# Performance work log

Measured on AMD Instinct MI355X. Metric: run time of the kernel, lower is better.

The kernel has to match this reference:

```python
import jax, jax.numpy as jnp
import numpy as np

HEAD_SIZE = 16
HIDDEN = 1024
NEG_INF = -1e9


def setup_inputs() -> dict:
    key = jax.random.key(0)
    ks = jax.random.split(key, 9)
    B, S, H = 2, 2048, HIDDEN
    q = jax.random.normal(ks[0], (B, S, H), dtype=jnp.float32)
    k = jax.random.normal(ks[1], (B, S, H), dtype=jnp.float32)
    v = jax.random.normal(ks[2], (B, S, H), dtype=jnp.float32)
    mask = jnp.ones((B, S), dtype=jnp.int32)
    scale = 1.0 / np.sqrt(H)
    wq = jax.random.normal(ks[3], (H, H), dtype=jnp.float32) * scale
    bq = jnp.zeros((H,), dtype=jnp.float32)
    wk = jax.random.normal(ks[4], (H, H), dtype=jnp.float32) * scale
    bk = jnp.zeros((H,), dtype=jnp.float32)
    wv = jax.random.normal(ks[5], (H, H), dtype=jnp.float32) * scale
    bv = jnp.zeros((H,), dtype=jnp.float32)
    return {"q": q, "k": k, "v": v, "mask": mask,
            "wq": wq, "bq": bq, "wk": wk, "bk": bk, "wv": wv, "bv": bv}


def _split_heads(x):
    # [B, S, H] -> [B, n_heads, S, head_dim]
    B, S, H = x.shape
    return x.reshape(B, S, HEAD_SIZE, H // HEAD_SIZE).transpose(0, 2, 1, 3)


def reference(q, k, v, mask, wq, bq, wk, bk, wv, bv):
    B, S, H = q.shape
    qh = _split_heads(q @ wq + bq)  # [B, nH, S, d]
    kh = _split_heads(k @ wk + bk)
    vh = _split_heads(v @ wv + bv)
    # scores scaled by sqrt(hidden_size) -- faithful to original (not head_dim)
    scores = jnp.einsum('bhqd,bhkd->bhqk', qh, kh) / jnp.sqrt(jnp.float32(H))
    # original: mask[0] of shape [B,S] -> [B,1,S,1], masks query rows
    m = mask.astype(jnp.float32)[:, None, :, None]  # [B,1,S,1]
    scores = scores + NEG_INF * (1.0 - m)
    weights = jax.nn.softmax(scores, axis=-1)
    out = jnp.einsum('bhqk,bhkd->bhqd', weights, vh)  # [B, nH, S, d]
    return out.transpose(0, 2, 1, 3).reshape(B, S, H)
```

## Files before the change

### kernel.cpp

```cpp
#include <hip/hip_runtime.h>
#include <hip/hip_bf16.h>
#include <math.h>

typedef __bf16 bf16_t;
typedef __bf16 bf16x8 __attribute__((ext_vector_type(8)));
typedef __bf16 bf16x4 __attribute__((ext_vector_type(4)));
typedef float floatx4 __attribute__((ext_vector_type(4)));

#define QSCALE 0.045084222f

__device__ __forceinline__ void gload_lds16(const bf16_t* g, bf16_t* l) {
  __builtin_amdgcn_global_load_lds(
      (const __attribute__((address_space(1))) void*)(g),
      (__attribute__((address_space(3))) void*)(l), 16, 0, 0);
}

__device__ __forceinline__ float fast_exp2(float x) {
  float r;
  asm("v_exp_f32 %0, %1" : "=v"(r) : "v"(x));
  return r;
}

__global__ __launch_bounds__(256) void transpose3_k(
    const float* __restrict__ wq, const float* __restrict__ wk,
    const float* __restrict__ wv, bf16_t* __restrict__ wt) {
  __shared__ float tile[32][33];
  const float* src = (blockIdx.z == 0) ? wq : (blockIdx.z == 1) ? wk : wv;
  bf16_t* dst = wt + (size_t)blockIdx.z * (1024u * 1024u);
  const int tx = threadIdx.x, ty = threadIdx.y;
  const int x = blockIdx.x * 32 + tx;
  const int y = blockIdx.y * 32 + ty;
#pragma unroll
  for (int i = 0; i < 32; i += 8)
    tile[ty + i][tx] = src[(size_t)(y + i) * 1024 + x];
  __syncthreads();
  const int x2 = blockIdx.y * 32 + tx;
  const int y2 = blockIdx.x * 32 + ty;
#pragma unroll
  for (int i = 0; i < 32; i += 8)
    dst[(size_t)(y2 + i) * 1024 + x2] = (bf16_t)tile[tx][ty + i];
}

__global__ __launch_bounds__(256) void qkv_gemm_k(
    const float* __restrict__ qx, const float* __restrict__ kx,
    const float* __restrict__ vx, const bf16_t* __restrict__ wt3,
    const float* __restrict__ bq, const float* __restrict__ bk,
    const float* __restrict__ bv, bf16_t* __restrict__ Qh,
    bf16_t* __restrict__ Kh, bf16_t* __restrict__ Vt) {
  const int proj = blockIdx.z;
  const float* X = (proj == 0) ? qx : (proj == 1) ? kx : vx;
  const bf16_t* Wt = wt3 + (size_t)proj * (1024u * 1024u);
  const float* bias = (proj == 0) ? bq : (proj == 1) ? bk : bv;

  __shared__ __align__(16) bf16_t As[128 * 64];
  __shared__ __align__(16) bf16_t Bs[128 * 64];

  const int t = threadIdx.x;
  const int lane = t & 63;
  const int w = t >> 6;
  const int wm = (w >> 1) * 64;
  const int wn = (w & 1) * 64;
  const int m0 = blockIdx.x * 128;
  const int n0 = blockIdx.y * 128;
  const int lm = lane & 15;
  const int lq = lane >> 4;

  floatx4 acc[4][4];
#pragma unroll
  for (int i = 0; i < 4; ++i)
#pragma unroll
    for (int j = 0; j < 4; ++j) acc[i][j] = (floatx4){0.f, 0.f, 0.f, 0.f};

  for (int k0 = 0; k0 < 1024; k0 += 64) {
    float4 fa[4][2];
#pragma unroll
    for (int c = 0; c < 4; ++c) {
      const int E = c * 2048 + t * 8;
      const int row = E >> 6;
      const int g = ((E >> 3) & 7) ^ (row & 7);
      const float* src = X + (size_t)(m0 + row) * 1024 + k0 + g * 8;
      fa[c][0] = *(const float4*)(src);
      fa[c][1] = *(const float4*)(src + 4);
    }
    __syncthreads();
#pragma unroll
    for (int c = 0; c < 4; ++c) {
      const int E = c * 2048 + t * 8;
      const int row = E >> 6;
      const int g = ((E >> 3) & 7) ^ (row & 7);
      gload_lds16(Wt + (size_t)(n0 + row) * 1024 + k0 + g * 8, Bs + E);
      bf16x8 hv;
      hv[0] = (bf16_t)fa[c][0].x; hv[1] = (bf16_t)fa[c][0].y;
      hv[2] = (bf16_t)fa[c][0].z; hv[3] = (bf16_t)fa[c][0].w;
      hv[4] = (bf16_t)fa[c][1].x; hv[5] = (bf16_t)fa[c][1].y;
      hv[6] = (bf16_t)fa[c][1].z; hv[7] = (bf16_t)fa[c][1].w;
      *(bf16x8*)(As + E) = hv;
    }
    __syncthreads();

#pragma unroll
    for (int kc = 0; kc < 2; ++kc) {
      bf16x8 a[4], b[4];
#pragma unroll
      for (int i = 0; i < 4; ++i) {
        const int ch = ((kc * 4 + lq) ^ (lm & 7)) * 8;
        a[i] = *(const bf16x8*)(As + (wm + i * 16 + lm) * 64 + ch);
        b[i] = *(const bf16x8*)(Bs + (wn + i * 16 + lm) * 64 + ch);
      }
      if (proj < 2) {
#pragma unroll
        for (int i = 0; i < 4; ++i)
#pragma unroll
          for (int j = 0; j < 4; ++j)
            acc[i][j] = __builtin_amdgcn_mfma_f32_16x16x32_bf16(b[j], a[i],
                                                               acc[i][j], 0, 0, 0);
      } else {
#pragma unroll
        for (int i = 0; i < 4; ++i)
#pragma unroll
          for (int j = 0; j < 4; ++j)
            acc[i][j] = __builtin_amdgcn_mfma_f32_16x16x32_bf16(a[i], b[j],
                                                               acc[i][j], 0, 0, 0);
      }
    }
  }

  if (proj == 2) {
#pragma unroll
    for (int j = 0; j < 4; ++j) {
      const int gn = n0 + wn + j * 16 + lm;
      const float bval = bias[gn];
      const int h = gn >> 6, d = gn & 63;
#pragma unroll
      for (int i = 0; i < 4; ++i) {
        const int gm = m0 + wm + i * 16 + lq * 4;
        const int bb = gm >> 11, s0 = gm & 2047;
        bf16x4 pk;
#pragma unroll
        for (int ii = 0; ii < 4; ++ii) pk[ii] = (bf16_t)(acc[i][j][ii] + bval);
        *(bf16x4*)(Vt + (((size_t)bb * 16 + h) * 64 + d) * 2048 + s0) = pk;
      }
    }
  } else {
    bf16_t* outp = (proj == 0) ? Qh : Kh;
    const float scale = (proj == 0) ? QSCALE : 1.0f;
#pragma unroll
    for (int j = 0; j < 4; ++j) {
      const int nb = n0 + wn + j * 16 + lq * 4;
      float bs4[4];
#pragma unroll
      for (int ii = 0; ii < 4; ++ii) bs4[ii] = bias[nb + ii];
      const int h = nb >> 6, d0 = nb & 63;
#pragma unroll
      for (int i = 0; i < 4; ++i) {
        const int gm = m0 + wm + i * 16 + lm;
        const int bb = gm >> 11, s = gm & 2047;
        bf16x4 pk;
#pragma unroll
        for (int ii = 0; ii < 4; ++ii)
          pk[ii] = (bf16_t)((acc[i][j][ii] + bs4[ii]) * scale);
        *(bf16x4*)(outp + (((size_t)bb * 16 + h) * 2048 + s) * 64 + d0) = pk;
      }
    }
  }
}

__global__ __launch_bounds__(256) void attn_k(
    const bf16_t* __restrict__ Qh, const bf16_t* __restrict__ Kh,
    const bf16_t* __restrict__ Vt, float* __restrict__ out) {
  __shared__ __align__(16) bf16_t Ks[128 * 64];
  __shared__ __align__(16) bf16_t Vs[64 * 128];
  __shared__ __align__(16) bf16_t Ps[4][32 * 128];

  const int t = threadIdx.x;
  const int lane = t & 63;
  const int w = t >> 6;
  const int lm = lane & 15;
  const int lq = lane >> 4;
  const int b = blockIdx.x >> 4, h = blockIdx.x & 15;
  const int q0 = blockIdx.y * 128;
  const size_t bh = (size_t)b * 16 + h;
  const bf16_t* Qb = Qh + bh * (2048 * 64);
  const bf16_t* Kb = Kh + bh * (2048 * 64);
  const bf16_t* Vb = Vt + bh * (64 * 2048);

  bf16x8 qf[2][2];
#pragma unroll
  for (int im = 0; im < 2; ++im)
#pragma unroll
    for (int kc = 0; kc < 2; ++kc)
      qf[im][kc] = *(const bf16x8*)(Qb +
          (size_t)(q0 + w * 32 + im * 16 + lm) * 64 + kc * 32 + lq * 8);

  float lsum[2] = {0.f, 0.f};
  floatx4 accO[2][4];
#pragma unroll
  for (int im = 0; im < 2; ++im)
#pragma unroll
    for (int jd = 0; jd < 4; ++jd) accO[im][jd] = (floatx4){0.f, 0.f, 0.f, 0.f};

  for (int kt = 0; kt < 2048; kt += 128) {
    __syncthreads();
#pragma unroll
    for (int c = 0; c < 4; ++c) {
      const int e = c * 2048 + t * 8;
      const int key = e >> 6, gk = ((e >> 3) & 7) ^ (key & 7);
      gload_lds16(Kb + (size_t)(kt + key) * 64 + gk * 8, Ks + e);
      const int vr = e >> 7, gv = ((e >> 3) & 15) ^ (vr & 15);
      gload_lds16(Vb + (size_t)vr * 2048 + kt + gv * 8, Vs + e);
    }
    __syncthreads();

    floatx4 accS[2][8];
#pragma unroll
    for (int jn = 0; jn < 8; ++jn) {
      const int krow = jn * 16 + lm;
      const bf16x8 k0 = *(const bf16x8*)(Ks + krow * 64 + ((lq) ^ (lm & 7)) * 8);
      const bf16x8 k1 = *(const bf16x8*)(Ks + krow * 64 + ((4 + lq) ^ (lm & 7)) * 8);
#pragma unroll
      for (int im = 0; im < 2; ++im) {
        floatx4 z = {0.f, 0.f, 0.f, 0.f};
        z = __builtin_amdgcn_mfma_f32_16x16x32_bf16(k0, qf[im][0], z, 0, 0, 0);
        z = __builtin_amdgcn_mfma_f32_16x16x32_bf16(k1, qf[im][1], z, 0, 0, 0);
        accS[im][jn] = z;
      }
    }

#pragma unroll
    for (int im = 0; im < 2; ++im) {
      const int pr = im * 16 + lm;
#pragma unroll
      for (int jn = 0; jn < 8; ++jn) {
        bf16x4 pk;
#pragma unroll
        for (int ii = 0; ii < 4; ++ii) {
          const float p = fast_exp2(accS[im][jn][ii]);
          lsum[im] += p;
          pk[ii] = (bf16_t)p;
        }
        const int c2 = ((jn * 2) + (lq >> 1)) ^ lm;
        *(bf16x4*)(Ps[w] + pr * 128 + c2 * 8 + (lq & 1) * 4) = pk;
      }
    }
    asm volatile("s_waitcnt lgkmcnt(0)" ::: "memory");

#pragma unroll
    for (int kc = 0; kc < 4; ++kc) {
      bf16x8 ap[2];
#pragma unroll
      for (int im = 0; im < 2; ++im)
        ap[im] = *(const bf16x8*)(Ps[w] + (im * 16 + lm) * 128 +
                                  ((kc * 4 + lq) ^ lm) * 8);
#pragma unroll
      for (int jd = 0; jd < 4; ++jd) {
        const bf16x8 vf = *(const bf16x8*)(Vs + (jd * 16 + lm) * 128 +
                                           ((kc * 4 + lq) ^ lm) * 8);
#pragma unroll
        for (int im = 0; im < 2; ++im)
          accO[im][jd] =
              __builtin_amdgcn_mfma_f32_16x16x32_bf16(vf, ap[im], accO[im][jd], 0, 0, 0);
      }
    }
  }

  float inv[2];
#pragma unroll
  for (int im = 0; im < 2; ++im) {
    float l = lsum[im];
    l += __shfl_xor(l, 16, 64);
    l += __shfl_xor(l, 32, 64);
    inv[im] = 1.0f / l;
  }

#pragma unroll
  for (int im = 0; im < 2; ++im) {
    const int s = q0 + w * 32 + im * 16 + lm;
    float* op = out + ((size_t)b * 2048 + s) * 1024 + h * 64 + lq * 4;
#pragma unroll
    for (int jd = 0; jd < 4; ++jd) {
      float4 o;
      o.x = accO[im][jd][0] * inv[im];
      o.y = accO[im][jd][1] * inv[im];
      o.z = accO[im][jd][2] * inv[im];
      o.w = accO[im][jd][3] * inv[im];
      *(float4*)(op + jd * 16) = o;
    }
  }
}

extern "C" void kernel_launch(void* const* d_in, const int* in_sizes, int n_in,
                              void* d_out, int out_size, void* d_ws, size_t ws_size,
                              hipStream_t stream) {
  (void)in_sizes; (void)n_in; (void)out_size; (void)ws_size;
  const float* q = (const float*)d_in[0];
  const float* k = (const float*)d_in[1];
  const float* v = (const float*)d_in[2];
  const float* wq = (const float*)d_in[4];
  const float* bq = (const float*)d_in[5];
  const float* wk = (const float*)d_in[6];
  const float* bk = (const float*)d_in[7];
  const float* wv = (const float*)d_in[8];
  const float* bv = (const float*)d_in[9];
  float* out = (float*)d_out;

  bf16_t* ws = (bf16_t*)d_ws;
  bf16_t* Wt = ws;
  bf16_t* Qh = ws + 3u * 1048576u;
  bf16_t* Kh = Qh + 4194304u;
  bf16_t* Vt = Kh + 4194304u;

  transpose3_k<<<dim3(32, 32, 3), dim3(32, 8, 1), 0, stream>>>(wq, wk, wv, Wt);
  qkv_gemm_k<<<dim3(32, 8, 3), dim3(256, 1, 1), 0, stream>>>(
      q, k, v, Wt, bq, bk, bv, Qh, Kh, Vt);
  attn_k<<<dim3(32, 16, 1), dim3(256, 1, 1), 0, stream>>>(Qh, Kh, Vt, out);
}
```

Baseline: 214.6 us.

## Double-buffer QKV GEMM tiles and register-prefetch K/V in attention loop

The projection GEMM now keeps two LDS buffers for A and B. It prefetches the next B tile by async global-to-LDS and the A tile two steps ahead into registers, so only one barrier is needed per iteration and loads overlap the MFMA work. The attention kernel replaces the direct global-to-LDS K/V loads with a register prefetch of the next tile, which is issued after the LDS store and runs during compute. The cost is twice the LDS in the GEMM and more registers in both kernels, which could lower occupancy.

```diff
diff --git a/kernel.cpp b/kernel.cpp
--- a/kernel.cpp
+++ b/kernel.cpp
@@ -52,8 +52,8 @@
   const bf16_t* Wt = wt3 + (size_t)proj * (1024u * 1024u);
   const float* bias = (proj == 0) ? bq : (proj == 1) ? bk : bv;
 
-  __shared__ __align__(16) bf16_t As[128 * 64];
-  __shared__ __align__(16) bf16_t Bs[128 * 64];
+  __shared__ __align__(16) bf16_t As[2][128 * 64];
+  __shared__ __align__(16) bf16_t Bs[2][128 * 64];
 
   const int t = threadIdx.x;
   const int lane = t & 63;
@@ -65,38 +65,63 @@
   const int lm = lane & 15;
   const int lq = lane >> 4;
 
+  int srow[4], sg[4];
+#pragma unroll
+  for (int c = 0; c < 4; ++c) {
+    const int E = c * 2048 + t * 8;
+    srow[c] = E >> 6;
+    sg[c] = (((E >> 3) & 7) ^ (srow[c] & 7)) * 8;
+  }
+
   floatx4 acc[4][4];
 #pragma unroll
   for (int i = 0; i < 4; ++i)
 #pragma unroll
     for (int j = 0; j < 4; ++j) acc[i][j] = (floatx4){0.f, 0.f, 0.f, 0.f};
 
-  for (int k0 = 0; k0 < 1024; k0 += 64) {
-    float4 fa[4][2];
-#pragma unroll
-    for (int c = 0; c < 4; ++c) {
-      const int E = c * 2048 + t * 8;
-      const int row = E >> 6;
-      const int g = ((E >> 3) & 7) ^ (row & 7);
-      const float* src = X + (size_t)(m0 + row) * 1024 + k0 + g * 8;
-      fa[c][0] = *(const float4*)(src);
-      fa[c][1] = *(const float4*)(src + 4);
-    }
+  float4 fa[2][4][2];
+
+#define LOAD_A(bank, k0)                                                     \
+  {                                                                          \
+    _Pragma("unroll") for (int c = 0; c < 4; ++c) {                          \
+      const float* src = X + (size_t)(m0 + srow[c]) * 1024 + (k0) + sg[c];   \
+      fa[bank][c][0] = *(const float4*)(src);                                \
+      fa[bank][c][1] = *(const float4*)(src + 4);                            \
+    }                                                                        \
+  }
+
+#define GLDS_B(buf, k0)                                                      \
+  {                                                                          \
+    _Pragma("unroll") for (int c = 0; c < 4; ++c) {                          \
+      const int E = c * 2048 + t * 8;                                        \
+      gload_lds16(Wt + (size_t)(n0 + srow[c]) * 1024 + (k0) + sg[c],         \
+                  Bs[buf] + E);                                              \
+    }                                                                        \
+  }
+
+#define CVT_WRITE_A(bank, buf)                                               \
+  {                                                                          \
+    _Pragma("unroll") for (int c = 0; c < 4; ++c) {                          \
+      const int E = c * 2048 + t * 8;                                        \
+      bf16x8 hv;                                                             \
+      hv[0] = (bf16_t)fa[bank][c][0].x; hv[1] = (bf16_t)fa[bank][c][0].y;    \
+      hv[2] = (bf16_t)fa[bank][c][0].z; hv[3] = (bf16_t)fa[bank][c][0].w;    \
+      hv[4] = (bf16_t)fa[bank][c][1].x; hv[5] = (bf16_t)fa[bank][c][1].y;    \
+      hv[6] = (bf16_t)fa[bank][c][1].z; hv[7] = (bf16_t)fa[bank][c][1].w;    \
+      *(bf16x8*)(As[buf] + E) = hv;                                          \
+    }                                                                        \
+  }
+
+  LOAD_A(0, 0);
+  GLDS_B(0, 0);
+  CVT_WRITE_A(0, 0);
+  LOAD_A(1, 64);
+
+  int p = 0;
+  for (int it = 0; it < 16; ++it, p ^= 1) {
     __syncthreads();
-#pragma unroll
-    for (int c = 0; c < 4; ++c) {
-      const int E = c * 2048 + t * 8;
-      const int row = E >> 6;
-      const int g = ((E >> 3) & 7) ^ (row & 7);
-      gload_lds16(Wt + (size_t)(n0 + row) * 1024 + k0 + g * 8, Bs + E);
-      bf16x8 hv;
-      hv[0] = (bf16_t)fa[c][0].x; hv[1] = (bf16_t)fa[c][0].y;
-      hv[2] = (bf16_t)fa[c][0].z; hv[3] = (bf16_t)fa[c][0].w;
-      hv[4] = (bf16_t)fa[c][1].x; hv[5] = (bf16_t)fa[c][1].y;
-      hv[6] = (bf16_t)fa[c][1].z; hv[7] = (bf16_t)fa[c][1].w;
-      *(bf16x8*)(As + E) = hv;
-    }
-    __syncthreads();
+    if (it + 1 < 16) GLDS_B(p ^ 1, (it + 1) * 64);
+    if (it + 2 < 16) LOAD_A(p, (it + 2) * 64);
 
 #pragma unroll
     for (int kc = 0; kc < 2; ++kc) {
@@ -104,8 +129,8 @@
 #pragma unroll
       for (int i = 0; i < 4; ++i) {
         const int ch = ((kc * 4 + lq) ^ (lm & 7)) * 8;
-        a[i] = *(const bf16x8*)(As + (wm + i * 16 + lm) * 64 + ch);
-        b[i] = *(const bf16x8*)(Bs + (wn + i * 16 + lm) * 64 + ch);
+        a[i] = *(const bf16x8*)(As[p] + (wm + i * 16 + lm) * 64 + ch);
+        b[i] = *(const bf16x8*)(Bs[p] + (wn + i * 16 + lm) * 64 + ch);
       }
       if (proj < 2) {
 #pragma unroll
@@ -123,7 +148,11 @@
                                                                acc[i][j], 0, 0, 0);
       }
     }
-  }
+    if (it + 1 < 16) CVT_WRITE_A(p ^ 1, p ^ 1);
+  }
+#undef LOAD_A
+#undef GLDS_B
+#undef CVT_WRITE_A
 
   if (proj == 2) {
 #pragma unroll
@@ -199,17 +228,32 @@
 #pragma unroll
     for (int jd = 0; jd < 4; ++jd) accO[im][jd] = (floatx4){0.f, 0.f, 0.f, 0.f};
 
+  bf16x8 kv[8];
+
+#define LOAD_KV(kt)                                                          \
+  {                                                                          \
+    _Pragma("unroll") for (int c = 0; c < 4; ++c) {                          \
+      const int e = c * 2048 + t * 8;                                        \
+      const int key = e >> 6, gk = ((e >> 3) & 7) ^ (key & 7);               \
+      kv[c] = *(const bf16x8*)(Kb + (size_t)((kt) + key) * 64 + gk * 8);     \
+      const int vr = e >> 7, gv = ((e >> 3) & 15) ^ (vr & 15);               \
+      kv[4 + c] = *(const bf16x8*)(Vb + (size_t)vr * 2048 + (kt) + gv * 8);  \
+    }                                                                        \
+  }
+
+  LOAD_KV(0);
+
   for (int kt = 0; kt < 2048; kt += 128) {
     __syncthreads();
 #pragma unroll
     for (int c = 0; c < 4; ++c) {
       const int e = c * 2048 + t * 8;
-      const int key = e >> 6, gk = ((e >> 3) & 7) ^ (key & 7);
-      gload_lds16(Kb + (size_t)(kt + key) * 64 + gk * 8, Ks + e);
-      const int vr = e >> 7, gv = ((e >> 3) & 15) ^ (vr & 15);
-      gload_lds16(Vb + (size_t)vr * 2048 + kt + gv * 8, Vs + e);
+      *(bf16x8*)(Ks + e) = kv[c];
+      *(bf16x8*)(Vs + e) = kv[4 + c];
     }
     __syncthreads();
+
+    if (kt + 128 < 2048) LOAD_KV(kt + 128);
 
     floatx4 accS[2][8];
 #pragma unroll
@@ -262,6 +306,7 @@
       }
     }
   }
+#undef LOAD_KV
 
   float inv[2];
 #pragma unroll
```

Result: slower. 327.4 us (+52.5%).

## Pre-convert activations to bf16 and register-prefetch K/V tiles in attention

Applied to the files above, without the earlier changes.

Adds a separate kernel that converts the q/k/v activations to bf16 once, so the QKV GEMM can load both operands straight into LDS with direct global-to-LDS loads instead of fp32 loads and per-tile conversion. The attention kernel now prefetches the next K/V tile into registers while computing the current one, then stores it to LDS, replacing the synchronous direct-to-LDS loads. The costs are an extra kernel launch with a full read and write of the activations, plus higher register pressure in the attention kernel.

```diff
diff --git a/kernel.cpp b/kernel.cpp
--- a/kernel.cpp
+++ b/kernel.cpp
@@ -19,6 +19,22 @@
   float r;
   asm("v_exp_f32 %0, %1" : "=v"(r) : "v"(x));
   return r;
+}
+
+__global__ __launch_bounds__(256) void cvt3_k(
+    const float* __restrict__ q, const float* __restrict__ k,
+    const float* __restrict__ v, bf16_t* __restrict__ xb) {
+  const float* src = (blockIdx.y == 0) ? q : (blockIdx.y == 1) ? k : v;
+  bf16_t* dst = xb + (size_t)blockIdx.y * 4194304u;
+  const int i = (blockIdx.x * 256 + threadIdx.x) * 8;
+  float4 f0 = *(const float4*)(src + i);
+  float4 f1 = *(const float4*)(src + i + 4);
+  bf16x8 hv;
+  hv[0] = (bf16_t)f0.x; hv[1] = (bf16_t)f0.y;
+  hv[2] = (bf16_t)f0.z; hv[3] = (bf16_t)f0.w;
+  hv[4] = (bf16_t)f1.x; hv[5] = (bf16_t)f1.y;
+  hv[6] = (bf16_t)f1.z; hv[7] = (bf16_t)f1.w;
+  *(bf16x8*)(dst + i) = hv;
 }
 
 __global__ __launch_bounds__(256) void transpose3_k(
@@ -42,14 +58,13 @@
 }
 
 __global__ __launch_bounds__(256) void qkv_gemm_k(
-    const float* __restrict__ qx, const float* __restrict__ kx,
-    const float* __restrict__ vx, const bf16_t* __restrict__ wt3,
+    const bf16_t* __restrict__ xb3, const bf16_t* __restrict__ wt3,
     const float* __restrict__ bq, const float* __restrict__ bk,
     const float* __restrict__ bv, bf16_t* __restrict__ Qh,
     bf16_t* __restrict__ Kh, bf16_t* __restrict__ Vt) {
   const int proj = blockIdx.z;
-  const float* X = (proj == 0) ? qx : (proj == 1) ? kx : vx;
-  const bf16_t* Wt = wt3 + (size_t)proj * (1024u * 1024u);
+  const bf16_t* X = xb3 + (size_t)proj * 4194304u;
+  const bf16_t* Wt = wt3 + (size_t)proj * 1048576u;
   const float* bias = (proj == 0) ? bq : (proj == 1) ? bk : bv;
 
   __shared__ __align__(16) bf16_t As[128 * 64];
@@ -65,6 +80,14 @@
   const int lm = lane & 15;
   const int lq = lane >> 4;
 
+  int srow[4], sg[4];
+#pragma unroll
+  for (int c = 0; c < 4; ++c) {
+    const int E = c * 2048 + t * 8;
+    srow[c] = E >> 6;
+    sg[c] = (((E >> 3) & 7) ^ (srow[c] & 7)) * 8;
+  }
+
   floatx4 acc[4][4];
 #pragma unroll
   for (int i = 0; i < 4; ++i)
@@ -72,29 +95,12 @@
     for (int j = 0; j < 4; ++j) acc[i][j] = (floatx4){0.f, 0.f, 0.f, 0.f};
 
   for (int k0 = 0; k0 < 1024; k0 += 64) {
-    float4 fa[4][2];
+    __syncthreads();
 #pragma unroll
     for (int c = 0; c < 4; ++c) {
       const int E = c * 2048 + t * 8;
-      const int row = E >> 6;
-      const int g = ((E >> 3) & 7) ^ (row & 7);
-      const float* src = X + (size_t)(m0 + row) * 1024 + k0 + g * 8;
-      fa[c][0] = *(const float4*)(src);
-      fa[c][1] = *(const float4*)(src + 4);
-    }
-    __syncthreads();
-#pragma unroll
-    for (int c = 0; c < 4; ++c) {
-      const int E = c * 2048 + t * 8;
-      const int row = E >> 6;
-      const int g = ((E >> 3) & 7) ^ (row & 7);
-      gload_lds16(Wt + (size_t)(n0 + row) * 1024 + k0 + g * 8, Bs + E);
-      bf16x8 hv;
-      hv[0] = (bf16_t)fa[c][0].x; hv[1] = (bf16_t)fa[c][0].y;
-      hv[2] = (bf16_t)fa[c][0].z; hv[3] = (bf16_t)fa[c][0].w;
-      hv[4] = (bf16_t)fa[c][1].x; hv[5] = (bf16_t)fa[c][1].y;
-      hv[6] = (bf16_t)fa[c][1].z; hv[7] = (bf16_t)fa[c][1].w;
-      *(bf16x8*)(As + E) = hv;
+      gload_lds16(X + (size_t)(m0 + srow[c]) * 1024 + k0 + sg[c], As + E);
+      gload_lds16(Wt + (size_t)(n0 + srow[c]) * 1024 + k0 + sg[c], Bs + E);
     }
     __syncthreads();
 
@@ -199,17 +205,32 @@
 #pragma unroll
     for (int jd = 0; jd < 4; ++jd) accO[im][jd] = (floatx4){0.f, 0.f, 0.f, 0.f};
 
+  bf16x8 kv[8];
+
+#define LOAD_KV(kt)                                                          \
+  {                                                                          \
+    _Pragma("unroll") for (int c = 0; c < 4; ++c) {                          \
+      const int e = c * 2048 + t * 8;                                        \
+      const int key = e >> 6, gk = ((e >> 3) & 7) ^ (key & 7);               \
+      kv[c] = *(const bf16x8*)(Kb + (size_t)((kt) + key) * 64 + gk * 8);     \
+      const int vr = e >> 7, gv = ((e >> 3) & 15) ^ (vr & 15);               \
+      kv[4 + c] = *(const bf16x8*)(Vb + (size_t)vr * 2048 + (kt) + gv * 8);  \
+    }                                                                        \
+  }
+
+  LOAD_KV(0);
+
   for (int kt = 0; kt < 2048; kt += 128) {
     __syncthreads();
 #pragma unroll
     for (int c = 0; c < 4; ++c) {
       const int e = c * 2048 + t * 8;
-      const int key = e >> 6, gk = ((e >> 3) & 7) ^ (key & 7);
-      gload_lds16(Kb + (size_t)(kt + key) * 64 + gk * 8, Ks + e);
-      const int vr = e >> 7, gv = ((e >> 3) & 15) ^ (vr & 15);
-      gload_lds16(Vb + (size_t)vr * 2048 + kt + gv * 8, Vs + e);
+      *(bf16x8*)(Ks + e) = kv[c];
+      *(bf16x8*)(Vs + e) = kv[4 + c];
     }
     __syncthreads();
+
+    if (kt + 128 < 2048) LOAD_KV(kt + 128);
 
     floatx4 accS[2][8];
 #pragma unroll
@@ -262,6 +283,7 @@
       }
     }
   }
+#undef LOAD_KV
 
   float inv[2];
 #pragma unroll
@@ -304,13 +326,15 @@
   float* out = (float*)d_out;
 
   bf16_t* ws = (bf16_t*)d_ws;
-  bf16_t* Wt = ws;
-  bf16_t* Qh = ws + 3u * 1048576u;
+  bf16_t* Xb = ws;
+  bf16_t* Wt = ws + 12582912u;
+  bf16_t* Qh = Wt + 3145728u;
   bf16_t* Kh = Qh + 4194304u;
   bf16_t* Vt = Kh + 4194304u;
 
+  cvt3_k<<<dim3(2048, 3, 1), dim3(256, 1, 1), 0, stream>>>(q, k, v, Xb);
   transpose3_k<<<dim3(32, 32, 3), dim3(32, 8, 1), 0, stream>>>(wq, wk, wv, Wt);
   qkv_gemm_k<<<dim3(32, 8, 3), dim3(256, 1, 1), 0, stream>>>(
-      q, k, v, Wt, bq, bk, bv, Qh, Kh, Vt);
+      Xb, Wt, bq, bk, bv, Qh, Kh, Vt);
   attn_k<<<dim3(32, 16, 1), dim3(256, 1, 1), 0, stream>>>(Qh, Kh, Vt, out);
 }
```

Result: faster. 203.5 us (-5.2%).
